# Kernel tuning notes

Measured on AMD Instinct MI355X. Metric: run time of the kernel, lower is better.

The kernel has to match this reference:

```python
import jax, jax.numpy as jnp
import numpy as np

B, T, C = 4, 4096, 1024
H = 16
D = C // H
EPS = 1e-06


def setup_inputs() -> dict:
    key = jax.random.key(0)
    k1, k2, k3 = jax.random.split(key, 3)
    x = jax.random.normal(k1, (B, T, C), dtype=jnp.float32)
    Wqkv = jax.random.normal(k2, (3 * C, C), dtype=jnp.float32) * (1.0 / np.sqrt(C))
    Wproj = jax.random.normal(k3, (C, C), dtype=jnp.float32) * (1.0 / np.sqrt(C))
    bproj = jnp.zeros((C,), dtype=jnp.float32)
    return {"x": x, "Wqkv": Wqkv, "Wproj": Wproj, "bproj": bproj}


def _phi(x):
    # elu(x) + 1 kernel feature map (non-negative)
    return jax.nn.elu(x) + 1.0


def reference(x, Wqkv, Wproj, bproj):
    b, t, c = x.shape
    qkv = jnp.einsum('btc,ec->bte', x, Wqkv)              # (B,T,3C)
    qkv = qkv.reshape(b, t, 3, H, D)
    q, k, v = qkv[:, :, 0], qkv[:, :, 1], qkv[:, :, 2]     # (B,T,H,D)
    q = _phi(q)
    k = _phi(k)
    # kv state: sum over sequence of outer products k_d v_m -> (B,H,D,D)
    kv = jnp.einsum('bnhd,bnhm->bhdm', k, v)
    k_sum = k.sum(axis=1)                                  # (B,H,D)
    out = jnp.einsum('bnhd,bhdm->bnhm', q, kv)             # (B,T,H,D)
    normalizer = jnp.einsum('bnhd,bhd->bnh', q, k_sum) + EPS
    out = out / normalizer[..., None]
    out = out.reshape(b, t, c)
    out = jnp.einsum('btc,oc->bto', out, Wproj) + bproj
    return out
```

## Files before the change

### kernel.cpp

```cpp
#include <hip/hip_runtime.h>

typedef __bf16 bf16;
typedef bf16 bf16x8 __attribute__((ext_vector_type(8)));
typedef bf16 bf16x4 __attribute__((ext_vector_type(4)));
typedef float f32x4 __attribute__((ext_vector_type(4)));

#define B_ 4
#define T_ 4096
#define C_ 1024
#define EPS_ 1e-6f
#define KVTSTR 16448

typedef __attribute__((address_space(1))) const void* as1p;
typedef __attribute__((address_space(3))) void* as3p;

__global__ void cast_kernel(const float* __restrict__ in, bf16* __restrict__ out, int n8) {
  int i = blockIdx.x * blockDim.x + threadIdx.x;
  int stride = gridDim.x * blockDim.x;
  for (; i < n8; i += stride) {
    const float4* p = (const float4*)(in + (size_t)i * 8);
    float4 v0 = p[0];
    float4 v1 = p[1];
    bf16x8 o;
    o[0] = (bf16)v0.x; o[1] = (bf16)v0.y; o[2] = (bf16)v0.z; o[3] = (bf16)v0.w;
    o[4] = (bf16)v1.x; o[5] = (bf16)v1.y; o[6] = (bf16)v1.z; o[7] = (bf16)v1.w;
    *(bf16x8*)(out + (size_t)i * 8) = o;
  }
}

#define BM 256
#define BN 256
#define BK 32
#define KD 1024
#define NT (KD / BK)
#define ABYT (BM * BK * 2)
#define BUFB (2 * ABYT)
#define SMEMB (4 * BUFB)

#define GSTEP(CURA, CURB, NXTA, NXTB, T)                                                       \
  do {                                                                                         \
    const bool st = (T) + 3 < NT;                                                              \
    if (st) {                                                                                  \
      const int ko = ((T) + 3) * BK;                                                           \
      char* db = smem + (((T) + 3) & 3) * BUFB;                                                \
      __builtin_amdgcn_global_load_lds((as1p)(pA0 + ko), (as3p)(db + tid * 16), 16, 0, 0);     \
      __builtin_amdgcn_global_load_lds((as1p)(pA1 + ko), (as3p)(db + 8192 + tid * 16), 16, 0, 0);   \
      __builtin_amdgcn_global_load_lds((as1p)(pB0 + ko), (as3p)(db + 16384 + tid * 16), 16, 0, 0);  \
      __builtin_amdgcn_global_load_lds((as1p)(pB1 + ko), (as3p)(db + 24576 + tid * 16), 16, 0, 0);  \
    }                                                                                          \
    if ((T) + 1 < NT) {                                                                        \
      const bf16* Ab = (const bf16*)(smem + (((T) + 1) & 3) * BUFB);                           \
      const bf16* Bb = Ab + BM * BK;                                                           \
      _Pragma("unroll") for (int mi = 0; mi < 8; mi++)                                         \
          NXTA[mi] = *(const bf16x8*)(Ab + (wm * 128 + mi * 16 + fr) * 32 + fsw);              \
      _Pragma("unroll") for (int nj = 0; nj < 4; nj++)                                         \
          NXTB[nj] = *(const bf16x8*)(Bb + (wn * 64 + nj * 16 + fr) * 32 + fsw);               \
    }                                                                                          \
    __builtin_amdgcn_s_setprio(1);                                                             \
    _Pragma("unroll") for (int mi = 0; mi < 8; mi++)                                           \
        _Pragma("unroll") for (int nj = 0; nj < 4; nj++)                                       \
            acc[mi][nj] = __builtin_amdgcn_mfma_f32_16x16x32_bf16(CURA[mi], CURB[nj], acc[mi][nj], 0, 0, 0); \
    __builtin_amdgcn_s_setprio(0);                                                             \
    asm volatile("s_waitcnt lgkmcnt(0)" ::: "memory");                                         \
    if (st) asm volatile("s_waitcnt vmcnt(4)" ::: "memory");                                   \
    else    asm volatile("s_waitcnt vmcnt(0)" ::: "memory");                                   \
    __builtin_amdgcn_s_barrier();                                                              \
    __builtin_amdgcn_sched_barrier(0);                                                         \
  } while (0)

template <int MODE>
__global__ __launch_bounds__(512, 1) void gemm6(
    const bf16* __restrict__ A, const bf16* __restrict__ Bm,
    void* __restrict__ Cout, const float* __restrict__ bias,
    bf16* __restrict__ kvt, int M, int N, int tiles_n) {
  extern __shared__ char smem[];
  const int tid = threadIdx.x;
  const int l = tid & 63;
  const int w = tid >> 6;
  const int wm = w >> 2;
  const int wn = w & 3;

  const int cpx = gridDim.x >> 3;
  const int bid = (blockIdx.x & 7) * cpx + (blockIdx.x >> 3);
  const int tm = (bid / tiles_n) * BM;
  const int tn = (bid % tiles_n) * BN;

  const int srow = tid >> 2;
  const int g8 = ((tid & 3) ^ ((tid >> 3) & 3)) * 8;

  const bf16* pA0 = A + (size_t)(tm + srow) * KD + g8;
  const bf16* pA1 = A + (size_t)(tm + 128 + srow) * KD + g8;
  const bf16* pB0 = Bm + (size_t)(tn + srow) * KD + g8;
  const bf16* pB1 = Bm + (size_t)(tn + 128 + srow) * KD + g8;

  const int fr = l & 15;
  const int fc = l >> 4;
  const int fsw = (fc ^ ((fr >> 1) & 3)) * 8;

  f32x4 acc[8][4] = {};
  bf16x8 afA[8], bfA[4], afB[8], bfB[4];

#pragma unroll
  for (int kt = 0; kt < 3; kt++) {
    char* db = smem + kt * BUFB;
    __builtin_amdgcn_global_load_lds((as1p)(pA0 + kt * BK), (as3p)(db + tid * 16), 16, 0, 0);
    __builtin_amdgcn_global_load_lds((as1p)(pA1 + kt * BK), (as3p)(db + 8192 + tid * 16), 16, 0, 0);
    __builtin_amdgcn_global_load_lds((as1p)(pB0 + kt * BK), (as3p)(db + 16384 + tid * 16), 16, 0, 0);
    __builtin_amdgcn_global_load_lds((as1p)(pB1 + kt * BK), (as3p)(db + 24576 + tid * 16), 16, 0, 0);
  }
  asm volatile("s_waitcnt vmcnt(4)" ::: "memory");
  __builtin_amdgcn_s_barrier();
  __builtin_amdgcn_sched_barrier(0);

  {
    const bf16* Ab = (const bf16*)(smem);
    const bf16* Bb = Ab + BM * BK;
#pragma unroll
    for (int mi = 0; mi < 8; mi++)
      afA[mi] = *(const bf16x8*)(Ab + (wm * 128 + mi * 16 + fr) * 32 + fsw);
#pragma unroll
    for (int nj = 0; nj < 4; nj++)
      bfA[nj] = *(const bf16x8*)(Bb + (wn * 64 + nj * 16 + fr) * 32 + fsw);
  }
  asm volatile("s_waitcnt lgkmcnt(0)" ::: "memory");
  __builtin_amdgcn_sched_barrier(0);

  for (int t = 0; t < NT; t += 2) {
    GSTEP(afA, bfA, afB, bfB, t);
    GSTEP(afB, bfB, afA, bfA, t + 1);
  }

  const int crow0 = tm + wm * 128 + (l >> 4) * 4;
  const int ccol0 = tn + wn * 64 + (l & 15);
  if (MODE == 0) {
    if (tn < 1024) {
      bf16* qbuf = (bf16*)Cout;
#pragma unroll
      for (int mi = 0; mi < 8; mi++)
#pragma unroll
        for (int nj = 0; nj < 4; nj++) {
          const int col = ccol0 + nj * 16;
#pragma unroll
          for (int r = 0; r < 4; r++) {
            const int row = crow0 + mi * 16 + r;
            float v = acc[mi][nj][r];
            v = (v > 0.f) ? (v + 1.0f) : __expf(v);
            qbuf[(size_t)row * 1024 + col] = (bf16)v;
          }
        }
    } else {
#pragma unroll
      for (int mi = 0; mi < 8; mi++)
#pragma unroll
        for (int nj = 0; nj < 4; nj++) {
          const int colp = ccol0 + nj * 16 - 1024;
          const bool isk = (colp < 1024);
          bf16x4 pk;
#pragma unroll
          for (int r = 0; r < 4; r++) {
            float v = acc[mi][nj][r];
            if (isk) v = (v > 0.f) ? (v + 1.0f) : __expf(v);
            pk[r] = (bf16)v;
          }
          const int n0 = crow0 + mi * 16;
          *(bf16x4*)(kvt + (size_t)colp * KVTSTR + n0) = pk;
        }
    }
  } else {
    float* Cf = (float*)Cout;
#pragma unroll
    for (int mi = 0; mi < 8; mi++)
#pragma unroll
      for (int nj = 0; nj < 4; nj++) {
        const int col = ccol0 + nj * 16;
        const float bv = bias[col];
#pragma unroll
        for (int r = 0; r < 4; r++) {
          const int row = crow0 + mi * 16 + r;
          Cf[(size_t)row * N + col] = acc[mi][nj][r] + bv;
        }
      }
  }
}

__global__ __launch_bounds__(256) void kvgemm(const bf16* __restrict__ kvt,
                                              float* __restrict__ partial) {
  const int kc = blockIdx.x >> 6;
  const int bh = blockIdx.x & 63;
  const int b = bh >> 4, h = bh & 15;
  const int l = threadIdx.x & 63;
  const int w = threadIdx.x >> 6;

  const size_t nb = (size_t)b * 4096 + kc * 1024 + (l >> 4) * 8;
  const bf16* Ar = kvt + (size_t)(h * 64 + w * 16 + (l & 15)) * KVTSTR + nb;
  const bf16* Br = kvt + (size_t)(1024 + h * 64 + (l & 15)) * KVTSTR + nb;

  f32x4 acc[4] = {};
  float ks = 0.f;
  bf16x8 aC, bC[4], aN, bN[4];
  aC = *(const bf16x8*)Ar;
#pragma unroll
  for (int nj = 0; nj < 4; nj++) bC[nj] = *(const bf16x8*)(Br + (size_t)nj * 16 * KVTSTR);

  for (int it = 0; it < 32; ++it) {
    if (it + 1 < 32) {
      aN = *(const bf16x8*)(Ar + (it + 1) * 32);
#pragma unroll
      for (int nj = 0; nj < 4; nj++)
        bN[nj] = *(const bf16x8*)(Br + (size_t)nj * 16 * KVTSTR + (it + 1) * 32);
    }
#pragma unroll
    for (int i = 0; i < 8; i++) ks += (float)aC[i];
#pragma unroll
    for (int nj = 0; nj < 4; nj++)
      acc[nj] = __builtin_amdgcn_mfma_f32_16x16x32_bf16(aC, bC[nj], acc[nj], 0, 0, 0);
    aC = aN;
#pragma unroll
    for (int nj = 0; nj < 4; nj++) bC[nj] = bN[nj];
  }

  ks += __shfl_xor(ks, 16);
  ks += __shfl_xor(ks, 32);

  float* p = partial + (size_t)(kc * 64 + bh) * 4160;
#pragma unroll
  for (int nj = 0; nj < 4; nj++) {
    const int m = nj * 16 + (l & 15);
#pragma unroll
    for (int r = 0; r < 4; r++) {
      const int d = w * 16 + (l >> 4) * 4 + r;
      p[d * 64 + m] = acc[nj][r];
    }
  }
  if (l < 16) p[4096 + w * 16 + l] = ks;
}

__global__ void kv_finalize(const float* __restrict__ partial, bf16* __restrict__ kvb) {
  const int bh = blockIdx.x;
  for (int i = threadIdx.x; i < 80 * 64; i += 256) {
    const int row = i >> 6;
    const int dd = i & 63;
    float outv = 0.f;
    if (row < 64) {
      float s = 0.f;
#pragma unroll
      for (int kc = 0; kc < 4; kc++)
        s += partial[(size_t)(kc * 64 + bh) * 4160 + dd * 64 + row];
      outv = s;
    } else if (row < 66) {
      float s = 0.f;
#pragma unroll
      for (int kc = 0; kc < 4; kc++)
        s += partial[(size_t)(kc * 64 + bh) * 4160 + 4096 + dd];
      bf16 hi = (bf16)s;
      outv = (row == 64) ? (float)hi : (s - (float)hi);
    }
    kvb[(size_t)bh * 5120 + row * 64 + dd] = (bf16)outv;
  }
}

__global__ __launch_bounds__(256) void attn_mfma(const bf16* __restrict__ qbuf,
                                                 const bf16* __restrict__ kvb,
                                                 bf16* __restrict__ attn) {
  const int bh = blockIdx.x >> 4;
  const int tch = blockIdx.x & 15;
  const int b = bh >> 4;
  const int h = bh & 15;
  const int lane = threadIdx.x & 63;
  const int wave = threadIdx.x >> 6;
  const int t0 = tch * 256 + wave * 64;

  const bf16* kvp = kvb + (size_t)bh * 5120;
  bf16x8 bfrag[5][2];
#pragma unroll
  for (int j = 0; j < 5; j++)
#pragma unroll
    for (int kk = 0; kk < 2; kk++)
      bfrag[j][kk] = *(const bf16x8*)(kvp + (j * 16 + (lane & 15)) * 64 + kk * 32 + (lane >> 4) * 8);

  f32x4 acc[4][5] = {};
#pragma unroll
  for (int i = 0; i < 4; i++) {
    const int t = t0 + i * 16 + (lane & 15);
    const bf16* qp = qbuf + (size_t)(b * T_ + t) * 1024 + h * 64 + (lane >> 4) * 8;
    bf16x8 a0 = *(const bf16x8*)qp;
    bf16x8 a1 = *(const bf16x8*)(qp + 32);
#pragma unroll
    for (int j = 0; j < 5; j++) {
      acc[i][j] = __builtin_amdgcn_mfma_f32_16x16x32_bf16(a0, bfrag[j][0], acc[i][j], 0, 0, 0);
      acc[i][j] = __builtin_amdgcn_mfma_f32_16x16x32_bf16(a1, bfrag[j][1], acc[i][j], 0, 0, 0);
    }
  }

#pragma unroll
  for (int i = 0; i < 4; i++) {
#pragma unroll
    for (int r = 0; r < 4; r++) {
      float hi = __shfl(acc[i][4][r], (lane & 48));
      float lo = __shfl(acc[i][4][r], (lane & 48) + 1);
      float inv = 1.0f / (hi + lo + EPS_);
      const int t = t0 + i * 16 + (lane >> 4) * 4 + r;
      bf16* op = attn + (size_t)(b * T_ + t) * 1024 + h * 64 + (lane & 15);
#pragma unroll
      for (int j = 0; j < 4; j++)
        op[j * 16] = (bf16)(acc[i][j][r] * inv);
    }
  }
}

extern "C" void kernel_launch(void* const* d_in, const int* in_sizes, int n_in,
                              void* d_out, int out_size, void* d_ws, size_t ws_size,
                              hipStream_t stream) {
  const float* x = (const float*)d_in[0];
  const float* Wqkv = (const float*)d_in[1];
  const float* Wproj = (const float*)d_in[2];
  const float* bproj = (const float*)d_in[3];
  float* out = (float*)d_out;

  char* w = (char*)d_ws;
  bf16* xw = (bf16*)w;      w += (size_t)16777216 * 2;
  bf16* wqkv = (bf16*)w;    w += (size_t)3145728 * 2;
  bf16* wproj = (bf16*)w;   w += (size_t)1048576 * 2;
  bf16* qbuf = (bf16*)w;    w += (size_t)16384 * 1024 * 2;
  bf16* kvt = (bf16*)w;     w += (size_t)2048 * KVTSTR * 2;
  bf16* attnb = (bf16*)w;   w += (size_t)16384 * 1024 * 2;
  float* partial = (float*)w; w += (size_t)4 * 64 * 4160 * 4;
  bf16* kvb = (bf16*)w;

  (void)hipFuncSetAttribute((const void*)gemm6<0>,
      hipFuncAttributeMaxDynamicSharedMemorySize, SMEMB);
  (void)hipFuncSetAttribute((const void*)gemm6<1>,
      hipFuncAttributeMaxDynamicSharedMemorySize, SMEMB);

  cast_kernel<<<8192, 256, 0, stream>>>(x, xw, 16777216 / 8);
  cast_kernel<<<1536, 256, 0, stream>>>(Wqkv, wqkv, 3145728 / 8);
  cast_kernel<<<512, 256, 0, stream>>>(Wproj, wproj, 1048576 / 8);

  gemm6<0><<<768, 512, SMEMB, stream>>>(xw, wqkv, (void*)qbuf, nullptr, kvt, 16384, 3072, 12);

  kvgemm<<<256, 256, 0, stream>>>(kvt, partial);
  kv_finalize<<<64, 256, 0, stream>>>(partial, kvb);

  attn_mfma<<<64 * 16, 256, 0, stream>>>(qbuf, kvb, attnb);

  gemm6<1><<<256, 512, SMEMB, stream>>>(attnb, wproj, (void*)out, bproj, nullptr, 16384, 1024, 4);
}
```

Measured before the change: 228.3 us.

## Restructure bf16 GEMM to BK=64 double-buffered pipeline with interleaved LDS loads

Replaces the 4-stage BK=32 register-double-buffered GEMM mainloop with a 2-stage BK=64 LDS double buffer. Each K tile is split into four sub-phases that load two A fragments, compute, and interleave the next tile's global-to-LDS copies with barriers. An 8-way XOR swizzle suits the wider 64-element rows. The aim is fewer barriers per K and better overlap of loads with MFMA work, at the cost of more frequent intra-tile barriers and shallower prefetch depth.

```diff
diff --git a/kernel.cpp b/kernel.cpp
--- a/kernel.cpp
+++ b/kernel.cpp
@@ -30,46 +30,33 @@
 
 #define BM 256
 #define BN 256
-#define BK 32
+#define BK 64
 #define KD 1024
-#define NT (KD / BK)
-#define ABYT (BM * BK * 2)
-#define BUFB (2 * ABYT)
-#define SMEMB (4 * BUFB)
-
-#define GSTEP(CURA, CURB, NXTA, NXTB, T)                                                       \
-  do {                                                                                         \
-    const bool st = (T) + 3 < NT;                                                              \
-    if (st) {                                                                                  \
-      const int ko = ((T) + 3) * BK;                                                           \
-      char* db = smem + (((T) + 3) & 3) * BUFB;                                                \
-      __builtin_amdgcn_global_load_lds((as1p)(pA0 + ko), (as3p)(db + tid * 16), 16, 0, 0);     \
-      __builtin_amdgcn_global_load_lds((as1p)(pA1 + ko), (as3p)(db + 8192 + tid * 16), 16, 0, 0);   \
-      __builtin_amdgcn_global_load_lds((as1p)(pB0 + ko), (as3p)(db + 16384 + tid * 16), 16, 0, 0);  \
-      __builtin_amdgcn_global_load_lds((as1p)(pB1 + ko), (as3p)(db + 24576 + tid * 16), 16, 0, 0);  \
-    }                                                                                          \
-    if ((T) + 1 < NT) {                                                                        \
-      const bf16* Ab = (const bf16*)(smem + (((T) + 1) & 3) * BUFB);                           \
-      const bf16* Bb = Ab + BM * BK;                                                           \
-      _Pragma("unroll") for (int mi = 0; mi < 8; mi++)                                         \
-          NXTA[mi] = *(const bf16x8*)(Ab + (wm * 128 + mi * 16 + fr) * 32 + fsw);              \
-      _Pragma("unroll") for (int nj = 0; nj < 4; nj++)                                         \
-          NXTB[nj] = *(const bf16x8*)(Bb + (wn * 64 + nj * 16 + fr) * 32 + fsw);               \
-    }                                                                                          \
-    __builtin_amdgcn_s_setprio(1);                                                             \
-    _Pragma("unroll") for (int mi = 0; mi < 8; mi++)                                           \
-        _Pragma("unroll") for (int nj = 0; nj < 4; nj++)                                       \
-            acc[mi][nj] = __builtin_amdgcn_mfma_f32_16x16x32_bf16(CURA[mi], CURB[nj], acc[mi][nj], 0, 0, 0); \
-    __builtin_amdgcn_s_setprio(0);                                                             \
-    asm volatile("s_waitcnt lgkmcnt(0)" ::: "memory");                                         \
-    if (st) asm volatile("s_waitcnt vmcnt(4)" ::: "memory");                                   \
-    else    asm volatile("s_waitcnt vmcnt(0)" ::: "memory");                                   \
-    __builtin_amdgcn_s_barrier();                                                              \
-    __builtin_amdgcn_sched_barrier(0);                                                         \
-  } while (0)
+#define NTI (KD / BK)
+#define TILB 32768
+#define BUFB (2 * TILB)
+#define SMEMB (2 * BUFB)
+
+#define STG(p, ko, dst) __builtin_amdgcn_global_load_lds((as1p)((p) + (ko)), (as3p)(dst), 16, 0, 0)
+
+#define LDA(MI0)                                                                       \
+  _Pragma("unroll") for (int a = 0; a < 2; a++)                                        \
+    _Pragma("unroll") for (int kk = 0; kk < 2; kk++)                                   \
+      af[a][kk] = *(const bf16x8*)(Ab + (wm * 128 + ((MI0) + a) * 16 + fr) * 64 + swz[kk]);
+
+#define MM(MI0)                                                                        \
+  __builtin_amdgcn_s_setprio(1);                                                       \
+  _Pragma("unroll") for (int a = 0; a < 2; a++)                                        \
+    _Pragma("unroll") for (int nj = 0; nj < 4; nj++)                                   \
+      _Pragma("unroll") for (int kk = 0; kk < 2; kk++)                                 \
+        acc[(MI0) + a][nj] = __builtin_amdgcn_mfma_f32_16x16x32_bf16(af[a][kk], bfr[nj][kk], acc[(MI0) + a][nj], 0, 0, 0); \
+  __builtin_amdgcn_s_setprio(0);
+
+#define BAR1 { __builtin_amdgcn_s_barrier(); asm volatile("s_waitcnt lgkmcnt(0)" ::: "memory"); __builtin_amdgcn_sched_barrier(0); }
+#define BAR2 { __builtin_amdgcn_s_barrier(); __builtin_amdgcn_sched_barrier(0); }
 
 template <int MODE>
-__global__ __launch_bounds__(512, 1) void gemm6(
+__global__ __launch_bounds__(512, 1) void gemm9(
     const bf16* __restrict__ A, const bf16* __restrict__ Bm,
     void* __restrict__ Cout, const float* __restrict__ bias,
     bf16* __restrict__ kvt, int M, int N, int tiles_n) {
@@ -85,49 +72,76 @@
   const int tm = (bid / tiles_n) * BM;
   const int tn = (bid % tiles_n) * BN;
 
-  const int srow = tid >> 2;
-  const int g8 = ((tid & 3) ^ ((tid >> 3) & 3)) * 8;
-
-  const bf16* pA0 = A + (size_t)(tm + srow) * KD + g8;
-  const bf16* pA1 = A + (size_t)(tm + 128 + srow) * KD + g8;
-  const bf16* pB0 = Bm + (size_t)(tn + srow) * KD + g8;
-  const bf16* pB1 = Bm + (size_t)(tn + 128 + srow) * KD + g8;
+  const int gsw = ((tid & 7) ^ ((tid >> 3) & 7)) * 8;
+  const int tsr = tid >> 3;
+
+  const bf16* pA0 = A + (size_t)(tm + tsr) * KD + gsw;
+  const bf16* pA1 = A + (size_t)(tm + 64 + tsr) * KD + gsw;
+  const bf16* pA2 = A + (size_t)(tm + 128 + tsr) * KD + gsw;
+  const bf16* pA3 = A + (size_t)(tm + 192 + tsr) * KD + gsw;
+  const bf16* pB0 = Bm + (size_t)(tn + tsr) * KD + gsw;
+  const bf16* pB1 = Bm + (size_t)(tn + 64 + tsr) * KD + gsw;
+  const bf16* pB2 = Bm + (size_t)(tn + 128 + tsr) * KD + gsw;
+  const bf16* pB3 = Bm + (size_t)(tn + 192 + tsr) * KD + gsw;
 
   const int fr = l & 15;
   const int fc = l >> 4;
-  const int fsw = (fc ^ ((fr >> 1) & 3)) * 8;
+  int swz[2];
+  swz[0] = ((0 * 4 + fc) ^ (fr & 7)) * 8;
+  swz[1] = ((1 * 4 + fc) ^ (fr & 7)) * 8;
 
   f32x4 acc[8][4] = {};
-  bf16x8 afA[8], bfA[4], afB[8], bfB[4];
-
-#pragma unroll
-  for (int kt = 0; kt < 3; kt++) {
-    char* db = smem + kt * BUFB;
-    __builtin_amdgcn_global_load_lds((as1p)(pA0 + kt * BK), (as3p)(db + tid * 16), 16, 0, 0);
-    __builtin_amdgcn_global_load_lds((as1p)(pA1 + kt * BK), (as3p)(db + 8192 + tid * 16), 16, 0, 0);
-    __builtin_amdgcn_global_load_lds((as1p)(pB0 + kt * BK), (as3p)(db + 16384 + tid * 16), 16, 0, 0);
-    __builtin_amdgcn_global_load_lds((as1p)(pB1 + kt * BK), (as3p)(db + 24576 + tid * 16), 16, 0, 0);
-  }
-  asm volatile("s_waitcnt vmcnt(4)" ::: "memory");
+
+  STG(pA0, 0, smem + tid * 16);
+  STG(pA1, 0, smem + 8192 + tid * 16);
+  STG(pA2, 0, smem + 16384 + tid * 16);
+  STG(pA3, 0, smem + 24576 + tid * 16);
+  STG(pB0, 0, smem + TILB + tid * 16);
+  STG(pB1, 0, smem + TILB + 8192 + tid * 16);
+  STG(pB2, 0, smem + TILB + 16384 + tid * 16);
+  STG(pB3, 0, smem + TILB + 24576 + tid * 16);
+  asm volatile("s_waitcnt vmcnt(0)" ::: "memory");
   __builtin_amdgcn_s_barrier();
   __builtin_amdgcn_sched_barrier(0);
 
-  {
-    const bf16* Ab = (const bf16*)(smem);
-    const bf16* Bb = Ab + BM * BK;
-#pragma unroll
-    for (int mi = 0; mi < 8; mi++)
-      afA[mi] = *(const bf16x8*)(Ab + (wm * 128 + mi * 16 + fr) * 32 + fsw);
+  for (int t = 0; t < NTI; ++t) {
+    const bf16* Ab = (const bf16*)(smem + (t & 1) * BUFB);
+    const bf16* Bb = (const bf16*)(smem + (t & 1) * BUFB + TILB);
+    char* sd = smem + ((t & 1) ^ 1) * BUFB;
+    const bool st = (t + 1 < NTI);
+    const int ko = (t + 1) * BK;
+    bf16x8 bfr[4][2], af[2][2];
+
 #pragma unroll
     for (int nj = 0; nj < 4; nj++)
-      bfA[nj] = *(const bf16x8*)(Bb + (wn * 64 + nj * 16 + fr) * 32 + fsw);
-  }
-  asm volatile("s_waitcnt lgkmcnt(0)" ::: "memory");
-  __builtin_amdgcn_sched_barrier(0);
-
-  for (int t = 0; t < NT; t += 2) {
-    GSTEP(afA, bfA, afB, bfB, t);
-    GSTEP(afB, bfB, afA, bfA, t + 1);
+#pragma unroll
+      for (int kk = 0; kk < 2; kk++)
+        bfr[nj][kk] = *(const bf16x8*)(Bb + (wn * 64 + nj * 16 + fr) * 64 + swz[kk]);
+    LDA(0)
+    if (st) {
+      STG(pB0, ko, sd + TILB + tid * 16);
+      STG(pB1, ko, sd + TILB + 8192 + tid * 16);
+      STG(pB2, ko, sd + TILB + 16384 + tid * 16);
+      STG(pB3, ko, sd + TILB + 24576 + tid * 16);
+    }
+    BAR1 MM(0) BAR2
+
+    LDA(2)
+    if (st) {
+      STG(pA0, ko, sd + tid * 16);
+      STG(pA1, ko, sd + 8192 + tid * 16);
+      STG(pA2, ko, sd + 16384 + tid * 16);
+      STG(pA3, ko, sd + 24576 + tid * 16);
+    }
+    BAR1 MM(2) BAR2
+
+    LDA(4)
+    BAR1 MM(4) BAR2
+
+    LDA(6)
+    BAR1 MM(6)
+    asm volatile("s_waitcnt vmcnt(0)" ::: "memory");
+    BAR2
   }
 
   const int crow0 = tm + wm * 128 + (l >> 4) * 4;
@@ -327,21 +341,21 @@
   float* partial = (float*)w; w += (size_t)4 * 64 * 4160 * 4;
   bf16* kvb = (bf16*)w;
 
-  (void)hipFuncSetAttribute((const void*)gemm6<0>,
+  (void)hipFuncSetAttribute((const void*)gemm9<0>,
       hipFuncAttributeMaxDynamicSharedMemorySize, SMEMB);
-  (void)hipFuncSetAttribute((const void*)gemm6<1>,
+  (void)hipFuncSetAttribute((const void*)gemm9<1>,
       hipFuncAttributeMaxDynamicSharedMemorySize, SMEMB);
 
   cast_kernel<<<8192, 256, 0, stream>>>(x, xw, 16777216 / 8);
   cast_kernel<<<1536, 256, 0, stream>>>(Wqkv, wqkv, 3145728 / 8);
   cast_kernel<<<512, 256, 0, stream>>>(Wproj, wproj, 1048576 / 8);
 
-  gemm6<0><<<768, 512, SMEMB, stream>>>(xw, wqkv, (void*)qbuf, nullptr, kvt, 16384, 3072, 12);
+  gemm9<0><<<768, 512, SMEMB, stream>>>(xw, wqkv, (void*)qbuf, nullptr, kvt, 16384, 3072, 12);
 
   kvgemm<<<256, 256, 0, stream>>>(kvt, partial);
   kv_finalize<<<64, 256, 0, stream>>>(partial, kvb);
 
   attn_mfma<<<64 * 16, 256, 0, stream>>>(qbuf, kvb, attnb);
 
-  gemm6<1><<<256, 512, SMEMB, stream>>>(attnb, wproj, (void*)out, bproj, nullptr, 16384, 1024, 4);
-}
+  gemm9<1><<<256, 512, SMEMB, stream>>>(attnb, wproj, (void*)out, bproj, nullptr, 16384, 1024, 4);
+}
```

Result: no change. 228.3 us (+0.0%).
